# Performance work log

Measured on AMD Instinct MI355X. Metric: run time of the kernel, lower is better.

## Reference

```python
import jax, jax.numpy as jnp
import numpy as np

N_HEAD = 16
D_HEAD = 64
D_MODEL = 1024
D_INNER = 4096
QLEN = 1024
MLEN = 1024
BSZ = 2
LN_EPS = 1e-5


def _layer_norm(x, g, b, eps=LN_EPS):
    mu = jnp.mean(x, axis=-1, keepdims=True)
    var = jnp.var(x, axis=-1, keepdims=True)
    return (x - mu) * jax.lax.rsqrt(var + eps) * g + b


def _rel_shift(x):
    # x: [qlen, rlen, bsz, n_head]
    q, r, b, n = x.shape
    zp = jnp.zeros((q, 1, b, n), x.dtype)
    xp = jnp.concatenate([zp, x], axis=1).reshape(r + 1, q, b, n)
    return xp[1:].reshape(q, r, b, n)


def setup_inputs() -> dict:
    key = jax.random.key(0)
    ks = jax.random.split(key, 12)
    klen = MLEN + QLEN
    w = jax.random.normal(ks[0], (QLEN, BSZ, D_MODEL), jnp.float32)
    r = jax.random.normal(ks[1], (klen, D_MODEL), jnp.float32)
    mems = jax.random.normal(ks[2], (MLEN, BSZ, D_MODEL), jnp.float32)
    # causal mask: query i attends keys j <= i + mlen
    i = jnp.arange(QLEN)[:, None]
    j = jnp.arange(klen)[None, :]
    attn_mask = (j > i + MLEN)[:, :, None]  # [qlen, klen, 1] bool
    s = 0.02
    params = dict(
        qkv_w=jax.random.normal(ks[3], (3 * N_HEAD * D_HEAD, D_MODEL), jnp.float32) * s,
        r_net_w=jax.random.normal(ks[4], (N_HEAD * D_HEAD, D_MODEL), jnp.float32) * s,
        o_w=jax.random.normal(ks[5], (D_MODEL, N_HEAD * D_HEAD), jnp.float32) * s,
        r_r_bias=jax.random.normal(ks[6], (N_HEAD, D_HEAD), jnp.float32) * s,
        r_w_bias=jax.random.normal(ks[7], (N_HEAD, D_HEAD), jnp.float32) * s,
        ln1_g=jnp.ones((D_MODEL,), jnp.float32),
        ln1_b=jnp.zeros((D_MODEL,), jnp.float32),
        ff_w1=jax.random.normal(ks[8], (D_INNER, D_MODEL), jnp.float32) * s,
        ff_b1=jnp.zeros((D_INNER,), jnp.float32),
        ff_w2=jax.random.normal(ks[9], (D_MODEL, D_INNER), jnp.float32) * s,
        ff_b2=jnp.zeros((D_MODEL,), jnp.float32),
        ln2_g=jnp.ones((D_MODEL,), jnp.float32),
        ln2_b=jnp.zeros((D_MODEL,), jnp.float32),
    )
    return dict(w=w, r=r, mems=mems, attn_mask=attn_mask, **params)


def reference(w, r, mems, attn_mask, qkv_w, r_net_w, o_w, r_r_bias, r_w_bias,
              ln1_g, ln1_b, ff_w1, ff_b1, ff_w2, ff_b2, ln2_g, ln2_b):
    qlen, bsz = w.shape[0], w.shape[1]
    scale = 1.0 / (D_HEAD ** 0.5)
    cat = jnp.concatenate([mems, w], axis=0)              # [klen, b, d_model]
    klen = cat.shape[0]
    w_heads = cat @ qkv_w.T                                # [klen, b, 3*n*d]
    wq, wk, wv = jnp.split(w_heads, 3, axis=-1)
    wq = wq[-qlen:]
    r_head_k = (r @ r_net_w.T).reshape(-1, N_HEAD, D_HEAD)  # [rlen, n, d]
    wq = wq.reshape(qlen, bsz, N_HEAD, D_HEAD)
    wk = wk.reshape(klen, bsz, N_HEAD, D_HEAD)
    wv = wv.reshape(klen, bsz, N_HEAD, D_HEAD)
    AC = jnp.einsum('ibnd,jbnd->ijbn', wq + r_w_bias, wk)   # content term
    BD = jnp.einsum('ibnd,jnd->ijbn', wq + r_r_bias, r_head_k)
    BD = _rel_shift(BD)                                     # position term
    attn_score = (AC + BD) * scale
    mask_value = jnp.finfo(attn_score.dtype).min
    attn_score = jnp.where(attn_mask[:, :, :, None], mask_value, attn_score)
    attn_prob = jax.nn.softmax(attn_score, axis=1)
    attn_vec = jnp.einsum('ijbn,jbnd->ibnd', attn_prob, wv)
    attn_vec = attn_vec.reshape(qlen, bsz, N_HEAD * D_HEAD)
    attn_out = attn_vec @ o_w.T
    h = _layer_norm(w + attn_out, ln1_g, ln1_b)             # post-lnorm
    core = jax.nn.relu(h @ ff_w1.T + ff_b1) @ ff_w2.T + ff_b2
    out = _layer_norm(h + core, ln2_g, ln2_b)
    return out
```

## Files before the change

### kernel.cpp

```cpp
#include <hip/hip_runtime.h>
#include <math.h>

#define QLEN 1024
#define MLEN 1024
#define KLEN 2048
#define BSZc 2
#define NH 16
#define DH 64
#define DM 1024
#define DI 4096

typedef unsigned short ushort_t;
typedef __attribute__((ext_vector_type(8))) short short8;
typedef __attribute__((ext_vector_type(4))) float f32x4;

__device__ __forceinline__ ushort_t f2bf(float x) {
    unsigned int u = __float_as_uint(x);
    unsigned int r = (u + 0x7FFFu + ((u >> 16) & 1u)) >> 16;
    return (ushort_t)r;
}

__device__ __forceinline__ void gload_lds16(const ushort_t* g, ushort_t* l) {
    __builtin_amdgcn_global_load_lds(
        (const __attribute__((address_space(1))) unsigned int*)g,
        (__attribute__((address_space(3))) unsigned int*)l,
        16, 0, 0);
}

__global__ __launch_bounds__(256)
void castbf(const float* __restrict__ s, ushort_t* __restrict__ d, int n)
{
    const int i = (blockIdx.x * 256 + threadIdx.x) * 8;
    if (i >= n) return;
    const float4 a = *(const float4*)(s + i);
    const float4 b = *(const float4*)(s + i + 4);
    short8 o;
    o[0] = (short)f2bf(a.x); o[1] = (short)f2bf(a.y);
    o[2] = (short)f2bf(a.z); o[3] = (short)f2bf(a.w);
    o[4] = (short)f2bf(b.x); o[5] = (short)f2bf(b.y);
    o[6] = (short)f2bf(b.z); o[7] = (short)f2bf(b.w);
    *(short8*)(d + i) = o;
}

template<int EMODE, int ACT, int BN>
__global__ __launch_bounds__(256)
void gemm_mfma(const ushort_t* __restrict__ A, const ushort_t* __restrict__ B,
               const float* __restrict__ bias,
               void* __restrict__ O0, void* __restrict__ O1,
               void* __restrict__ O2, void* __restrict__ O3,
               const float* __restrict__ rwb, const float* __restrict__ rrb,
               int M, int N, int K)
{
    constexpr int JT = BN / 32;
    __shared__ ushort_t At[128 * 32];
    __shared__ ushort_t Bt[BN * 32];

    const int tid  = threadIdx.x;
    const int lane = tid & 63;
    const int w    = tid >> 6;
    const int lr   = lane & 15;
    const int quad = lane >> 4;
    const int m0   = blockIdx.x * 128;
    const int n0   = blockIdx.y * BN;
    const int wm0  = (w >> 1) * 64;
    const int wn0  = (w & 1) * (BN / 2);

    f32x4 acc[4][JT];
#pragma unroll
    for (int it = 0; it < 4; ++it)
#pragma unroll
        for (int jt = 0; jt < JT; ++jt) acc[it][jt] = (f32x4){0.f, 0.f, 0.f, 0.f};

    const int srow = lane >> 2;
    const int scol = (lane & 3) << 3;
    const ushort_t* Ag = A + (size_t)(m0 + w * 32 + srow) * K + scol;
    ushort_t* lA0 = At + (w * 32) * 32;
    ushort_t* lA1 = At + (w * 32 + 16) * 32;
    const ushort_t* Bg;
    ushort_t *lB0, *lB1 = nullptr;
    if (BN == 128) {
        Bg  = B + (size_t)(n0 + w * 32 + srow) * K + scol;
        lB0 = Bt + (w * 32) * 32;
        lB1 = Bt + (w * 32 + 16) * 32;
    } else {
        Bg  = B + (size_t)(n0 + w * 16 + srow) * K + scol;
        lB0 = Bt + (w * 16) * 32;
    }

    const ushort_t* Ato = At + (wm0 + lr) * 32 + quad * 8;
    const ushort_t* Bto = Bt + (wn0 + lr) * 32 + quad * 8;

    for (int k0 = 0; k0 < K; k0 += 32) {
        __syncthreads();
        gload_lds16(Ag + k0, lA0);
        gload_lds16(Ag + (size_t)16 * K + k0, lA1);
        gload_lds16(Bg + k0, lB0);
        if (BN == 128) gload_lds16(Bg + (size_t)16 * K + k0, lB1);
        __syncthreads();

        short8 af[4], bf[JT];
#pragma unroll
        for (int it = 0; it < 4; ++it)
            af[it] = *(const short8*)(Ato + it * 16 * 32);
#pragma unroll
        for (int jt = 0; jt < JT; ++jt)
            bf[jt] = *(const short8*)(Bto + jt * 16 * 32);
#pragma unroll
        for (int it = 0; it < 4; ++it)
#pragma unroll
            for (int jt = 0; jt < JT; ++jt)
                acc[it][jt] = __builtin_amdgcn_mfma_f32_16x16x32_bf16(
                    af[it], bf[jt], acc[it][jt], 0, 0, 0);
    }

#pragma unroll
    for (int it = 0; it < 4; ++it)
#pragma unroll
        for (int jt = 0; jt < JT; ++jt)
#pragma unroll
            for (int rg = 0; rg < 4; ++rg) {
                const int m = m0 + wm0 + it * 16 + quad * 4 + rg;
                const int n = n0 + wn0 + jt * 16 + lr;
                float v = acc[it][jt][rg];
                if (EMODE == 0) {
                    if (bias) v += bias[n];
                    ((float*)O0)[(size_t)m * N + n] = v;
                } else if (EMODE == 1) {
                    const int j = m >> 1, b = m & 1;
                    const int part = n >> 10, hh = (n >> 6) & 15, d = n & 63;
                    if (part == 0) {
                        if (j >= MLEN) {
                            const int qi = j - MLEN;
                            const size_t qidx = (((size_t)(b * NH + hh)) * QLEN + qi) * DH + d;
                            ((ushort_t*)O0)[qidx] = f2bf(v + rwb[hh * DH + d]);
                            ((ushort_t*)O1)[qidx] = f2bf(v + rrb[hh * DH + d]);
                        }
                    } else if (part == 1) {
                        ((ushort_t*)O2)[(((size_t)(b * NH + hh)) * KLEN + j) * DH + d] = f2bf(v);
                    } else {
                        ((ushort_t*)O3)[(((size_t)(b * NH + hh)) * DH + d) * KLEN + j] = f2bf(v);
                    }
                } else if (EMODE == 2) {
                    const int hh = n >> 6, d = n & 63;
                    ((ushort_t*)O0)[(((size_t)hh) * KLEN + m) * DH + d] = f2bf(v);
                } else {
                    v += bias[n];
                    if (ACT == 1) v = fmaxf(v, 0.f);
                    ((ushort_t*)O0)[(size_t)m * N + n] = f2bf(v);
                }
            }
}

__global__ __launch_bounds__(256)
void attn_mfma(const ushort_t* __restrict__ Qac, const ushort_t* __restrict__ Qbd,
               const ushort_t* __restrict__ Kb, const ushort_t* __restrict__ Vt,
               const ushort_t* __restrict__ Rb, ushort_t* __restrict__ AV)
{
    __shared__ ushort_t Kt[64][72];
    __shared__ ushort_t Rt[128][72];
    __shared__ ushort_t Vl[64][72];
    __shared__ float    Bw[4][16][84];

    const int tid  = threadIdx.x;
    const int lane = tid & 63;
    const int w    = tid >> 6;
    const int lr   = lane & 15;
    const int quad = lane >> 4;
    const int bx   = blockIdx.x;
    const int i0   = bx << 6;
    const int bh   = blockIdx.y;
    const int h    = bh & 15;
    const int b    = bh >> 4;

    short8 qaf[2], qbf[2];
    {
        const size_t rowoff = ((size_t)bh * QLEN + i0 + w * 16 + lr) * DH;
#pragma unroll
        for (int kt = 0; kt < 2; ++kt) {
            qaf[kt] = *(const short8*)(Qac + rowoff + kt * 32 + quad * 8);
            qbf[kt] = *(const short8*)(Qbd + rowoff + kt * 32 + quad * 8);
        }
    }

    f32x4 O[4];
#pragma unroll
    for (int nt = 0; nt < 4; ++nt) O[nt] = (f32x4){0.f, 0.f, 0.f, 0.f};
    float m_run = -3.4e38f, l_run = 0.f;

    const int nc  = bx + 17;
    const int stw = 3 - w;
    const ushort_t* Kh = Kb + (size_t)bh * KLEN * DH;
    const ushort_t* Vh = Vt + (size_t)bh * DH * KLEN;
    const ushort_t* Rh = Rb + (size_t)h * KLEN * DH;

    for (int c = 0; c < nc; ++c) {
        const int j0 = c << 6;
        const int wb = 960 - i0 + j0;
        __syncthreads();
#pragma unroll
        for (int t = 0; t < 2; ++t) {
            int f = tid + (t << 8);
            int row = f >> 3, c8 = (f & 7) << 3;
            *(int4*)&Kt[row][c8] = *(const int4*)(Kh + (size_t)(j0 + row) * DH + c8);
        }
#pragma unroll
        for (int t = 0; t < 2; ++t) {
            int f = tid + (t << 8);
            int d = f >> 3, c8 = (f & 7) << 3;
            *(int4*)&Vl[d][c8] = *(const int4*)(Vh + (size_t)d * KLEN + j0 + c8);
        }
        {
            const int npass = (c == 0) ? 4 : 2;
            const int gb    = (c == 0) ? wb : wb + 64;
            for (int t = 0; t < npass; ++t) {
                int f = tid + (t << 8);
                int rl2 = f >> 3, c8 = (f & 7) << 3;
                int g = gb + rl2;
                int gc = g > (KLEN - 1) ? (KLEN - 1) : g;
                *(int4*)&Rt[g & 127][c8] = *(const int4*)(Rh + (size_t)gc * DH + c8);
            }
        }
        __syncthreads();

#pragma unroll
        for (int ctl = 0; ctl < 5; ++ctl) {
            const int wr = (stw + ctl) * 16 + lr;
            const int ring = (wb + wr) & 127;
            f32x4 z = (f32x4){0.f, 0.f, 0.f, 0.f};
#pragma unroll
            for (int kt = 0; kt < 2; ++kt) {
                short8 rb2 = *(const short8*)&Rt[ring][kt * 32 + quad * 8];
                z = __builtin_amdgcn_mfma_f32_16x16x32_bf16(qbf[kt], rb2, z, 0, 0, 0);
            }
#pragma unroll
            for (int rg = 0; rg < 4; ++rg)
                Bw[w][quad * 4 + rg][ctl * 16 + lr] = z[rg];
        }
#pragma unroll
        for (int ct = 0; ct < 4; ++ct) {
            f32x4 z = (f32x4){0.f, 0.f, 0.f, 0.f};
#pragma unroll
            for (int kt = 0; kt < 2; ++kt) {
                short8 kb2 = *(const short8*)&Kt[ct * 16 + lr][kt * 32 + quad * 8];
                z = __builtin_amdgcn_mfma_f32_16x16x32_bf16(qaf[kt], kb2, z, 0, 0, 0);
            }
#pragma unroll
            for (int rg = 0; rg < 4; ++rg) {
                const int rrow = quad * 4 + rg;
                Bw[w][rrow][ct * 16 + lr + 15 - rrow] += z[rg];
            }
        }

        const int lim = i0 + w * 16 + lr + 1024 - j0;
        float pv[16];
        float mx = -3.4e38f;
#pragma unroll
        for (int kt = 0; kt < 2; ++kt)
#pragma unroll
            for (int t = 0; t < 8; ++t) {
                const int jj = kt * 32 + quad * 8 + t;
                float s = Bw[w][lr][jj + 15 - lr] * 0.125f;
                s = (jj > lim) ? -3.4e38f : s;
                pv[kt * 8 + t] = s;
                mx = fmaxf(mx, s);
            }
        mx = fmaxf(mx, __shfl_xor(mx, 16, 64));
        mx = fmaxf(mx, __shfl_xor(mx, 32, 64));
        const float m_new = fmaxf(m_run, mx);
        float ps = 0.f;
        short8 pf[2];
#pragma unroll
        for (int kt = 0; kt < 2; ++kt)
#pragma unroll
            for (int t = 0; t < 8; ++t) {
                const float e = __expf(pv[kt * 8 + t] - m_new);
                ps += e;
                pf[kt][t] = (short)f2bf(e);
            }
        ps += __shfl_xor(ps, 16, 64);
        ps += __shfl_xor(ps, 32, 64);
        const float alpha = __expf(m_run - m_new);
        m_run = m_new;
        l_run = l_run * alpha + ps;

        float ar[4];
#pragma unroll
        for (int rg = 0; rg < 4; ++rg)
            ar[rg] = __shfl(alpha, quad * 4 + rg, 64);
#pragma unroll
        for (int nt = 0; nt < 4; ++nt) {
            O[nt][0] *= ar[0]; O[nt][1] *= ar[1];
            O[nt][2] *= ar[2]; O[nt][3] *= ar[3];
        }
#pragma unroll
        for (int kt = 0; kt < 2; ++kt)
#pragma unroll
            for (int nt = 0; nt < 4; ++nt) {
                short8 vb = *(const short8*)&Vl[nt * 16 + lr][kt * 32 + quad * 8];
                O[nt] = __builtin_amdgcn_mfma_f32_16x16x32_bf16(pf[kt], vb, O[nt], 0, 0, 0);
            }
    }

    float rlv[4];
#pragma unroll
    for (int rg = 0; rg < 4; ++rg)
        rlv[rg] = 1.f / __shfl(l_run, quad * 4 + rg, 64);
#pragma unroll
    for (int nt = 0; nt < 4; ++nt)
#pragma unroll
        for (int rg = 0; rg < 4; ++rg) {
            const int i = i0 + w * 16 + quad * 4 + rg;
            AV[((size_t)i * BSZc + b) * DM + h * DH + nt * 16 + lr] = f2bf(O[nt][rg] * rlv[rg]);
        }
}

__global__ __launch_bounds__(256)
void add_ln(const float* __restrict__ X, const float* __restrict__ Y,
            const float* __restrict__ gg, const float* __restrict__ bb,
            float* __restrict__ out, ushort_t* __restrict__ outb)
{
    const int row  = blockIdx.x;
    const int tid  = threadIdx.x;
    const int lane = tid & 63;
    const int w    = tid >> 6;
    __shared__ float ssum[4], ssq[4];

    const float4 xv = ((const float4*)(X + (size_t)row * DM))[tid];
    const float4 yv = ((const float4*)(Y + (size_t)row * DM))[tid];
    const float v0 = xv.x + yv.x, v1 = xv.y + yv.y;
    const float v2 = xv.z + yv.z, v3 = xv.w + yv.w;
    float s = v0 + v1 + v2 + v3;
    float q = v0 * v0 + v1 * v1 + v2 * v2 + v3 * v3;
#pragma unroll
    for (int off = 32; off > 0; off >>= 1) {
        s += __shfl_xor(s, off, 64);
        q += __shfl_xor(q, off, 64);
    }
    if (lane == 0) { ssum[w] = s; ssq[w] = q; }
    __syncthreads();
    s = ssum[0] + ssum[1] + ssum[2] + ssum[3];
    q = ssq[0] + ssq[1] + ssq[2] + ssq[3];
    const float mean = s * (1.f / DM);
    const float var  = q * (1.f / DM) - mean * mean;
    const float rs   = rsqrtf(var + 1e-5f);
    const float4 g4 = ((const float4*)gg)[tid];
    const float4 b4 = ((const float4*)bb)[tid];
    float4 ov;
    ov.x = (v0 - mean) * rs * g4.x + b4.x;
    ov.y = (v1 - mean) * rs * g4.y + b4.y;
    ov.z = (v2 - mean) * rs * g4.z + b4.z;
    ov.w = (v3 - mean) * rs * g4.w + b4.w;
    ((float4*)(out + (size_t)row * DM))[tid] = ov;
    if (outb) {
        ushort_t* p = outb + (size_t)row * DM + tid * 4;
        p[0] = f2bf(ov.x); p[1] = f2bf(ov.y);
        p[2] = f2bf(ov.z); p[3] = f2bf(ov.w);
    }
}

extern "C" void kernel_launch(void* const* d_in, const int* in_sizes, int n_in,
                              void* d_out, int out_size, void* d_ws, size_t ws_size,
                              hipStream_t stream)
{
    (void)in_sizes; (void)n_in; (void)out_size; (void)ws_size;
    const float* w      = (const float*)d_in[0];
    const float* r      = (const float*)d_in[1];
    const float* mems   = (const float*)d_in[2];
    const float* qkv_w  = (const float*)d_in[4];
    const float* rnet_w = (const float*)d_in[5];
    const float* o_w    = (const float*)d_in[6];
    const float* r_r_b  = (const float*)d_in[7];
    const float* r_w_b  = (const float*)d_in[8];
    const float* ln1g   = (const float*)d_in[9];
    const float* ln1b   = (const float*)d_in[10];
    const float* ffw1   = (const float*)d_in[11];
    const float* ffb1   = (const float*)d_in[12];
    const float* ffw2   = (const float*)d_in[13];
    const float* ffb2   = (const float*)d_in[14];
    const float* ln2g   = (const float*)d_in[15];
    const float* ln2b   = (const float*)d_in[16];
    float* out = (float*)d_out;

    char* wsb = (char*)d_ws;
    const size_t MB = 1024 * 1024;
    ushort_t* W1    = (ushort_t*)(wsb + 0 * MB);
    ushort_t* W2    = (ushort_t*)(wsb + 6 * MB);
    ushort_t* Acat  = (ushort_t*)(wsb + 8 * MB);
    ushort_t* Rsrc  = (ushort_t*)(wsb + 16 * MB);
    ushort_t* Qac   = (ushort_t*)(wsb + 20 * MB);
    ushort_t* Qbd   = (ushort_t*)(wsb + 24 * MB);
    ushort_t* Kbf   = (ushort_t*)(wsb + 28 * MB);
    ushort_t* Vt    = (ushort_t*)(wsb + 36 * MB);
    ushort_t* Rh    = (ushort_t*)(wsb + 44 * MB);
    ushort_t* AVec  = (ushort_t*)(wsb + 0 * MB);
    ushort_t* W3    = (ushort_t*)(wsb + 4 * MB);
    float*    AOut  = (float*)(wsb + 8 * MB);
    float*    Hbuf  = (float*)(wsb + 16 * MB);
    ushort_t* Hbf   = (ushort_t*)(wsb + 24 * MB);
    ushort_t* W4    = (ushort_t*)(wsb + 28 * MB);
    ushort_t* FFbf  = (ushort_t*)(wsb + 36 * MB);
    ushort_t* W5    = (ushort_t*)(wsb + 52 * MB);
    float*    Core  = (float*)(wsb + 0 * MB);

    dim3 blk(256);

    castbf<<<dim3(3145728 / 2048), blk, 0, stream>>>(qkv_w, W1, 3145728);
    castbf<<<dim3(1048576 / 2048), blk, 0, stream>>>(rnet_w, W2, 1048576);
    castbf<<<dim3(2097152 / 2048), blk, 0, stream>>>(mems, Acat, 2097152);
    castbf<<<dim3(2097152 / 2048), blk, 0, stream>>>(w, Acat + 2097152, 2097152);
    castbf<<<dim3(2097152 / 2048), blk, 0, stream>>>(r, Rsrc, 2097152);

    gemm_mfma<1, 0, 128><<<dim3(32, 24), blk, 0, stream>>>(
        Acat, W1, nullptr, Qac, Qbd, Kbf, Vt, r_w_b, r_r_b, 4096, 3072, 1024);

    gemm_mfma<2, 0, 64><<<dim3(16, 16), blk, 0, stream>>>(
        Rsrc, W2, nullptr, Rh, nullptr, nullptr, nullptr, nullptr, nullptr,
        2048, 1024, 1024);

    attn_mfma<<<dim3(QLEN / 64, BSZc * NH), blk, 0, stream>>>(
        Qac, Qbd, Kbf, Vt, Rh, AVec);

    castbf<<<dim3(1048576 / 2048), blk, 0, stream>>>(o_w, W3, 1048576);
    gemm_mfma<0, 0, 64><<<dim3(16, 16), blk, 0, stream>>>(
        AVec, W3, nullptr, AOut, nullptr, nullptr, nullptr, nullptr, nullptr,
        2048, 1024, 1024);

    add_ln<<<dim3(2 * QLEN), blk, 0, stream>>>(w, AOut, ln1g, ln1b, Hbuf, Hbf);

    castbf<<<dim3(4194304 / 2048), blk, 0, stream>>>(ffw1, W4, 4194304);
    gemm_mfma<3, 1, 128><<<dim3(16, 32), blk, 0, stream>>>(
        Hbf, W4, ffb1, FFbf, nullptr, nullptr, nullptr, nullptr, nullptr,
        2048, 4096, 1024);

    castbf<<<dim3(4194304 / 2048), blk, 0, stream>>>(ffw2, W5, 4194304);
    gemm_mfma<0, 0, 64><<<dim3(16, 16), blk, 0, stream>>>(
        FFbf, W5, ffb2, Core, nullptr, nullptr, nullptr, nullptr, nullptr,
        2048, 1024, 4096);

    add_ln<<<dim3(2 * QLEN), blk, 0, stream>>>(Hbuf, Core, ln2g, ln2b, out, nullptr);
}
```

Before: 461.4 us.

## Merge cast kernels, reverse query-tile order per batch, use bf16 score buffer and exp2

Fuses the eight separate fp32-to-bf16 cast launches into two multi-segment kernels, cutting launch count and tail gaps. In attention, blocks for the second batch walk query tiles in reverse so heavy and light causal tiles mix across the grid for better load balance. The score staging buffer in LDS is stored as bf16 instead of fp32, halving its footprint and bandwidth. Softmax switches to exp2 with log2e folded into the scale. The bf16 score accumulation loses precision before softmax, which risks accuracy.

```diff
diff --git a/kernel.cpp b/kernel.cpp
--- a/kernel.cpp
+++ b/kernel.cpp
@@ -19,6 +19,9 @@
     unsigned int r = (u + 0x7FFFu + ((u >> 16) & 1u)) >> 16;
     return (ushort_t)r;
 }
+__device__ __forceinline__ float bf2f(ushort_t b) {
+    return __uint_as_float(((unsigned int)b) << 16);
+}
 
 __device__ __forceinline__ void gload_lds16(const ushort_t* g, ushort_t* l) {
     __builtin_amdgcn_global_load_lds(
@@ -27,19 +30,42 @@
         16, 0, 0);
 }
 
-__global__ __launch_bounds__(256)
-void castbf(const float* __restrict__ s, ushort_t* __restrict__ d, int n)
-{
-    const int i = (blockIdx.x * 256 + threadIdx.x) * 8;
-    if (i >= n) return;
-    const float4 a = *(const float4*)(s + i);
-    const float4 b = *(const float4*)(s + i + 4);
+__device__ __forceinline__ void cast8(const float* s, ushort_t* d, int g) {
+    const float4 a = *(const float4*)(s + g * 8);
+    const float4 b = *(const float4*)(s + g * 8 + 4);
     short8 o;
     o[0] = (short)f2bf(a.x); o[1] = (short)f2bf(a.y);
     o[2] = (short)f2bf(a.z); o[3] = (short)f2bf(a.w);
     o[4] = (short)f2bf(b.x); o[5] = (short)f2bf(b.y);
     o[6] = (short)f2bf(b.z); o[7] = (short)f2bf(b.w);
-    *(short8*)(d + i) = o;
+    *(short8*)(d + g * 8) = o;
+}
+
+__global__ __launch_bounds__(256)
+void cast_phase1(const float* __restrict__ qkv_w, const float* __restrict__ rnet_w,
+                 const float* __restrict__ mems, const float* __restrict__ w,
+                 const float* __restrict__ r,
+                 ushort_t* __restrict__ W1, ushort_t* __restrict__ W2,
+                 ushort_t* __restrict__ Acat, ushort_t* __restrict__ Rsrc)
+{
+    int g = blockIdx.x * 256 + threadIdx.x;
+    if (g < 393216)            { cast8(qkv_w,  W1,              g); }
+    else if (g < 524288)       { cast8(rnet_w, W2,              g - 393216); }
+    else if (g < 786432)       { cast8(mems,   Acat,            g - 524288); }
+    else if (g < 1048576)      { cast8(w,      Acat + 2097152,  g - 786432); }
+    else if (g < 1310720)      { cast8(r,      Rsrc,            g - 1048576); }
+}
+
+__global__ __launch_bounds__(256)
+void cast_phase2(const float* __restrict__ o_w, const float* __restrict__ ffw1,
+                 const float* __restrict__ ffw2,
+                 ushort_t* __restrict__ W3, ushort_t* __restrict__ W4,
+                 ushort_t* __restrict__ W5)
+{
+    int g = blockIdx.x * 256 + threadIdx.x;
+    if (g < 131072)            { cast8(o_w,  W3, g); }
+    else if (g < 655360)       { cast8(ffw1, W4, g - 131072); }
+    else if (g < 1179648)      { cast8(ffw2, W5, g - 655360); }
 }
 
 template<int EMODE, int ACT, int BN>
@@ -159,16 +185,16 @@
     __shared__ ushort_t Kt[64][72];
     __shared__ ushort_t Rt[128][72];
     __shared__ ushort_t Vl[64][72];
-    __shared__ float    Bw[4][16][84];
+    __shared__ ushort_t Bw[4][16][84];
 
     const int tid  = threadIdx.x;
     const int lane = tid & 63;
     const int w    = tid >> 6;
     const int lr   = lane & 15;
     const int quad = lane >> 4;
-    const int bx   = blockIdx.x;
-    const int i0   = bx << 6;
     const int bh   = blockIdx.y;
+    const int qt   = (bh & 16) ? (15 - (int)blockIdx.x) : (int)blockIdx.x;
+    const int i0   = qt << 6;
     const int h    = bh & 15;
     const int b    = bh >> 4;
 
@@ -187,8 +213,9 @@
     for (int nt = 0; nt < 4; ++nt) O[nt] = (f32x4){0.f, 0.f, 0.f, 0.f};
     float m_run = -3.4e38f, l_run = 0.f;
 
-    const int nc  = bx + 17;
+    const int nc  = qt + 17;
     const int stw = 3 - w;
+    const float SC = 0.125f * 1.44269504f;
     const ushort_t* Kh = Kb + (size_t)bh * KLEN * DH;
     const ushort_t* Vh = Vt + (size_t)bh * DH * KLEN;
     const ushort_t* Rh = Rb + (size_t)h * KLEN * DH;
@@ -234,7 +261,7 @@
             }
 #pragma unroll
             for (int rg = 0; rg < 4; ++rg)
-                Bw[w][quad * 4 + rg][ctl * 16 + lr] = z[rg];
+                Bw[w][quad * 4 + rg][ctl * 16 + lr] = f2bf(z[rg]);
         }
 #pragma unroll
         for (int ct = 0; ct < 4; ++ct) {
@@ -247,7 +274,8 @@
 #pragma unroll
             for (int rg = 0; rg < 4; ++rg) {
                 const int rrow = quad * 4 + rg;
-                Bw[w][rrow][ct * 16 + lr + 15 - rrow] += z[rg];
+                ushort_t* p = &Bw[w][rrow][ct * 16 + lr + 15 - rrow];
+                *p = f2bf(bf2f(*p) + z[rg]);
             }
         }
 
@@ -259,7 +287,7 @@
 #pragma unroll
             for (int t = 0; t < 8; ++t) {
                 const int jj = kt * 32 + quad * 8 + t;
-                float s = Bw[w][lr][jj + 15 - lr] * 0.125f;
+                float s = bf2f(Bw[w][lr][jj + 15 - lr]) * SC;
                 s = (jj > lim) ? -3.4e38f : s;
                 pv[kt * 8 + t] = s;
                 mx = fmaxf(mx, s);
@@ -273,13 +301,13 @@
         for (int kt = 0; kt < 2; ++kt)
 #pragma unroll
             for (int t = 0; t < 8; ++t) {
-                const float e = __expf(pv[kt * 8 + t] - m_new);
+                const float e = exp2f(pv[kt * 8 + t] - m_new);
                 ps += e;
                 pf[kt][t] = (short)f2bf(e);
             }
         ps += __shfl_xor(ps, 16, 64);
         ps += __shfl_xor(ps, 32, 64);
-        const float alpha = __expf(m_run - m_new);
+        const float alpha = exp2f(m_run - m_new);
         m_run = m_new;
         l_run = l_run * alpha + ps;
 
@@ -404,11 +432,8 @@
 
     dim3 blk(256);
 
-    castbf<<<dim3(3145728 / 2048), blk, 0, stream>>>(qkv_w, W1, 3145728);
-    castbf<<<dim3(1048576 / 2048), blk, 0, stream>>>(rnet_w, W2, 1048576);
-    castbf<<<dim3(2097152 / 2048), blk, 0, stream>>>(mems, Acat, 2097152);
-    castbf<<<dim3(2097152 / 2048), blk, 0, stream>>>(w, Acat + 2097152, 2097152);
-    castbf<<<dim3(2097152 / 2048), blk, 0, stream>>>(r, Rsrc, 2097152);
+    cast_phase1<<<dim3(5120), blk, 0, stream>>>(qkv_w, rnet_w, mems, w, r,
+                                                W1, W2, Acat, Rsrc);
 
     gemm_mfma<1, 0, 128><<<dim3(32, 24), blk, 0, stream>>>(
         Acat, W1, nullptr, Qac, Qbd, Kbf, Vt, r_w_b, r_r_b, 4096, 3072, 1024);
@@ -420,19 +445,18 @@
     attn_mfma<<<dim3(QLEN / 64, BSZc * NH), blk, 0, stream>>>(
         Qac, Qbd, Kbf, Vt, Rh, AVec);
 
-    castbf<<<dim3(1048576 / 2048), blk, 0, stream>>>(o_w, W3, 1048576);
+    cast_phase2<<<dim3(4608), blk, 0, stream>>>(o_w, ffw1, ffw2, W3, W4, W5);
+
     gemm_mfma<0, 0, 64><<<dim3(16, 16), blk, 0, stream>>>(
         AVec, W3, nullptr, AOut, nullptr, nullptr, nullptr, nullptr, nullptr,
         2048, 1024, 1024);
 
     add_ln<<<dim3(2 * QLEN), blk, 0, stream>>>(w, AOut, ln1g, ln1b, Hbuf, Hbf);
 
-    castbf<<<dim3(4194304 / 2048), blk, 0, stream>>>(ffw1, W4, 4194304);
     gemm_mfma<3, 1, 128><<<dim3(16, 32), blk, 0, stream>>>(
         Hbf, W4, ffb1, FFbf, nullptr, nullptr, nullptr, nullptr, nullptr,
         2048, 4096, 1024);
 
-    castbf<<<dim3(4194304 / 2048), blk, 0, stream>>>(ffw2, W5, 4194304);
     gemm_mfma<0, 0, 64><<<dim3(16, 16), blk, 0, stream>>>(
         FFbf, W5, ffb2, Core, nullptr, nullptr, nullptr, nullptr, nullptr,
         2048, 1024, 4096);
```

Result: no change. 460.0 us (-0.3%).
